# Performance work log

Measured on AMD Instinct MI355X. Metric: run time of the kernel, lower is better.

## Reference

```python
import jax, jax.numpy as jnp
import numpy as np

B, D_IN, D_OUT, Q, NUM_CLASSES = 256, 512, 256, 16, 100
POOL = 2  # patch_size = sqrt(n=4) -> 2x2 spatial mean pooling


def setup_inputs() -> dict:
    key = jax.random.key(0)
    k1, k2, k3 = jax.random.split(key, 3)
    X = jax.random.normal(k1, (B, D_IN, Q), jnp.float32)
    # FRMap weight init: randn(d_out, d_in) / sqrt(d_in)
    W = jax.random.normal(k2, (D_OUT, D_IN), jnp.float32) / np.sqrt(D_IN)
    d2 = D_OUT // POOL
    fc_w = jax.random.normal(k3, (NUM_CLASSES, d2 * d2), jnp.float32) / np.sqrt(d2 * d2)
    fc_b = jnp.zeros((NUM_CLASSES,), jnp.float32)
    return {"X": X, "W": W, "fc_w": fc_w, "fc_b": fc_b}


def reference(X, W, fc_w, fc_b):
    # FRMap: Y = W @ X  -> (B, d_out, q)
    Y = jnp.einsum('oi,biq->boq', W, X)
    # ReOrth: Q from reduced QR of Y -> orthonormal (B, d_out, q)
    Qm, _ = jnp.linalg.qr(Y)
    # ProjMap: P = Q Q^T -> (B, d_out, d_out)
    P = jnp.einsum('biq,bjq->bij', Qm, Qm)
    # ProjPooling (spatial, n=4): 2x2 mean pooling == adaptive_avg_pool2d to (d/2, d/2)
    b, d, _ = P.shape
    d2 = d // POOL
    Pp = P.reshape(b, d2, POOL, d2, POOL).mean(axis=(2, 4))  # (B, d2, d2)
    # OrthMap: top-q eigenvectors of symmetric Pp (eigh ascending -> take last q, descending)
    _, V = jnp.linalg.eigh(Pp)
    U = V[..., ::-1][..., :Q]  # (B, d2, q)
    # OutputBlock: ProjMap + flatten + FC
    P2 = jnp.einsum('biq,bjq->bij', U, U)  # (B, d2, d2)
    logits = P2.reshape(b, -1) @ fc_w.T + fc_b  # (B, num_classes)
    return logits
```

## Files before the change

### kernel.cpp

```cpp
#include <hip/hip_runtime.h>
#include <hip/hip_bf16.h>
#include <cstdint>

#define BATCH 256
#define DIN   512
#define D2    128
#define NQ    16
#define NC    100
#define KFC   (D2 * D2)

#define KS    32
#define KCH   (KFC / KS)
#define STEPS (KCH / 32)

#define ZPAD  132
#define CVT_BLKS  800
#define W2_BLKS   256
#define BIAS_BLKS 100

typedef short short8 __attribute__((ext_vector_type(8)));
typedef float f32x4  __attribute__((ext_vector_type(4)));
typedef float f32x16 __attribute__((ext_vector_type(16)));

static __device__ __forceinline__ unsigned short f2bf_rne(float f) {
    unsigned x = __float_as_uint(f);
    return (unsigned short)((x + 0x7fffu + ((x >> 16) & 1u)) >> 16);
}
static __device__ __forceinline__ float bf2f(unsigned short u) {
    return __uint_as_float(((unsigned)u) << 16);
}

__global__ __launch_bounds__(256) void k_prep(const float* __restrict__ W,
                                              const float* __restrict__ fcw,
                                              const float* __restrict__ fcb,
                                              __hip_bfloat16* __restrict__ W2hi,
                                              __hip_bfloat16* __restrict__ W2lo,
                                              __hip_bfloat16* __restrict__ fcw16,
                                              float* __restrict__ out) {
    int blk = blockIdx.x;
    if (blk < CVT_BLKS) {
        int i = (blk * 256 + threadIdx.x) * 8;
        float4 a = *(const float4*)(fcw + i);
        float4 b = *(const float4*)(fcw + i + 4);
        short8 v;
        __hip_bfloat16* h = (__hip_bfloat16*)&v;
        h[0] = __float2bfloat16(a.x); h[1] = __float2bfloat16(a.y);
        h[2] = __float2bfloat16(a.z); h[3] = __float2bfloat16(a.w);
        h[4] = __float2bfloat16(b.x); h[5] = __float2bfloat16(b.y);
        h[6] = __float2bfloat16(b.z); h[7] = __float2bfloat16(b.w);
        *(short8*)(fcw16 + i) = v;
    } else if (blk < CVT_BLKS + W2_BLKS) {
        int idx = (blk - CVT_BLKS) * 256 + threadIdx.x;
        int o = idx >> 9;
        int i = idx & (DIN - 1);
        float v = 0.5f * (W[(size_t)(2 * o) * DIN + i] +
                          W[(size_t)(2 * o + 1) * DIN + i]);
        unsigned short hi = f2bf_rne(v);
        unsigned short lo = f2bf_rne(v - bf2f(hi));
        *(unsigned short*)(W2hi + idx) = hi;
        *(unsigned short*)(W2lo + idx) = lo;
    } else {
        int idx = (blk - CVT_BLKS - W2_BLKS) * 256 + threadIdx.x;
        int c = idx % NC;
        out[idx] = fcb[c];
    }
}

#define GJ_STEP(K) do {                                                   \
    float piv = __shfl(g[(K) & 7], ((K) >> 3) * 16 + (K), 64);            \
    float fac = __shfl(g[(K) & 7], ((K) >> 3) * 16 + r, 64);              \
    float inv = 1.0f / piv;                                               \
    float f   = fac * inv;                                                \
    float p0 = __shfl(g[0], cg16 + (K), 64);                              \
    float p1 = __shfl(g[1], cg16 + (K), 64);                              \
    float p2 = __shfl(g[2], cg16 + (K), 64);                              \
    float p3 = __shfl(g[3], cg16 + (K), 64);                              \
    float p4 = __shfl(g[4], cg16 + (K), 64);                              \
    float p5 = __shfl(g[5], cg16 + (K), 64);                              \
    float p6 = __shfl(g[6], cg16 + (K), 64);                              \
    float p7 = __shfl(g[7], cg16 + (K), 64);                              \
    bool isk = (r == (K));                                                \
    g[0] = isk ? p0 * inv : fmaf(-f, p0, g[0]);                           \
    g[1] = isk ? p1 * inv : fmaf(-f, p1, g[1]);                           \
    g[2] = isk ? p2 * inv : fmaf(-f, p2, g[2]);                           \
    g[3] = isk ? p3 * inv : fmaf(-f, p3, g[3]);                           \
    g[4] = isk ? p4 * inv : fmaf(-f, p4, g[4]);                           \
    g[5] = isk ? p5 * inv : fmaf(-f, p5, g[5]);                           \
    g[6] = isk ? p6 * inv : fmaf(-f, p6, g[6]);                           \
    g[7] = isk ? p7 * inv : fmaf(-f, p7, g[7]);                           \
} while (0)

__global__ __launch_bounds__(512) void k_zgep(const float* __restrict__ X,
                                              const __hip_bfloat16* __restrict__ W2hi,
                                              const __hip_bfloat16* __restrict__ W2lo,
                                              __hip_bfloat16* __restrict__ P2) {
    __shared__ float Xs[DIN][17];
    __shared__ unsigned int FragHi[16 * 256];
    __shared__ unsigned int FragLo[16 * 256];
    __shared__ float Zt[NQ][ZPAD];
    __shared__ float Et[NQ][ZPAD];
    __shared__ float Gi[NQ][36];

    int b = blockIdx.x;
    int t = threadIdx.x;
    int l = t & 63;
    int wv = t >> 6;

    {
        const float4* src = (const float4*)(X + (size_t)b * DIN * NQ);
        #pragma unroll
        for (int r = 0; r < 4; ++r) {
            float4 v = src[t + r * 512];
            int idx = (t + r * 512) * 4;
            int i = idx >> 4, q = idx & 15;
            Xs[i][q]     = v.x;
            Xs[i][q + 1] = v.y;
            Xs[i][q + 2] = v.z;
            Xs[i][q + 3] = v.w;
        }
    }
    __syncthreads();

    #pragma unroll
    for (int it = 0; it < 8; ++it) {
        int d  = t + it * 512;
        int s  = d >> 8;
        int ln = (d >> 2) & 63;
        int jj = d & 3;
        int q  = ln & 15;
        int i0 = s * 32 + ((ln >> 4) & 3) * 8 + jj * 2;
        float v0 = Xs[i0][q], v1 = Xs[i0 + 1][q];
        unsigned short h0 = f2bf_rne(v0), h1 = f2bf_rne(v1);
        unsigned short l0 = f2bf_rne(v0 - bf2f(h0));
        unsigned short l1 = f2bf_rne(v1 - bf2f(h1));
        FragHi[d] = (unsigned)h0 | ((unsigned)h1 << 16);
        FragLo[d] = (unsigned)l0 | ((unsigned)l1 << 16);
    }
    __syncthreads();

    {
        int m  = l & 15;
        int kg = (l >> 4) * 8;
        const __hip_bfloat16* whi = W2hi + (size_t)(wv * 16 + m) * DIN + kg;
        const __hip_bfloat16* wlo = W2lo + (size_t)(wv * 16 + m) * DIN + kg;
        f32x4 acc = {0.f, 0.f, 0.f, 0.f};
        #pragma unroll 4
        for (int s = 0; s < 16; ++s) {
            short8 ahi = *(const short8*)(whi + s * 32);
            short8 alo = *(const short8*)(wlo + s * 32);
            short8 bhi = *(const short8*)(&FragHi[s * 256 + l * 4]);
            short8 blo = *(const short8*)(&FragLo[s * 256 + l * 4]);
            acc = __builtin_amdgcn_mfma_f32_16x16x32_bf16(ahi, bhi, acc, 0, 0, 0);
            acc = __builtin_amdgcn_mfma_f32_16x16x32_bf16(ahi, blo, acc, 0, 0, 0);
            acc = __builtin_amdgcn_mfma_f32_16x16x32_bf16(alo, bhi, acc, 0, 0, 0);
        }
        int r0 = (l >> 4) * 4;
        #pragma unroll
        for (int j = 0; j < 4; ++j)
            Zt[m][wv * 16 + r0 + j] = acc[j];
    }
    __syncthreads();

    if (t < 256) {
        int qq = t >> 4, rr = t & 15;
        float s = 0.f;
        for (int i = 0; i < D2; i += 4) {
            float4 a = *(const float4*)&Zt[qq][i];
            float4 c = *(const float4*)&Zt[rr][i];
            s = fmaf(a.x, c.x, s); s = fmaf(a.y, c.y, s);
            s = fmaf(a.z, c.z, s); s = fmaf(a.w, c.w, s);
        }
        Gi[qq][rr] = s;
        Gi[qq][NQ + rr] = (qq == rr) ? 1.f : 0.f;
    }
    __syncthreads();

    if (t < 64) {
        int r    = t & 15;
        int cgg  = t >> 4;
        int cg16 = cgg * 16;
        float g[8];
        #pragma unroll
        for (int j = 0; j < 8; ++j) g[j] = Gi[r][cgg * 8 + j];
        GJ_STEP(0);  GJ_STEP(1);  GJ_STEP(2);  GJ_STEP(3);
        GJ_STEP(4);  GJ_STEP(5);  GJ_STEP(6);  GJ_STEP(7);
        GJ_STEP(8);  GJ_STEP(9);  GJ_STEP(10); GJ_STEP(11);
        GJ_STEP(12); GJ_STEP(13); GJ_STEP(14); GJ_STEP(15);
        if (cgg >= 2) {
            #pragma unroll
            for (int j = 0; j < 8; ++j) Gi[r][cgg * 8 + j] = g[j];
        }
    }
    __syncthreads();

    {
        int o  = t & (D2 - 1);
        int qg = (t >> 7) * 4;
        float acc[4] = {};
        #pragma unroll
        for (int rp = 0; rp < NQ; ++rp) {
            float z = Zt[rp][o];
            #pragma unroll
            for (int j = 0; j < 4; ++j)
                acc[j] = fmaf(z, Gi[rp][NQ + qg + j], acc[j]);
        }
        #pragma unroll
        for (int j = 0; j < 4; ++j) Et[qg + j][o] = acc[j];
    }
    __syncthreads();

    {
        __hip_bfloat16* P2b = P2 + (size_t)b * KFC;
        int ti = wv >> 1;
        int tj0 = (wv & 1) * 2;
        int r8 = (l >> 5) * 8;
        int rm = l & 31;

        short8 afr;
        {
            __hip_bfloat16* ah = (__hip_bfloat16*)&afr;
            #pragma unroll
            for (int j = 0; j < 8; ++j)
                ah[j] = __float2bfloat16(Et[r8 + j][ti * 32 + rm]);
        }
        #pragma unroll
        for (int tjo = 0; tjo < 2; ++tjo) {
            int tj = tj0 + tjo;
            short8 bfr;
            __hip_bfloat16* bh = (__hip_bfloat16*)&bfr;
            #pragma unroll
            for (int j = 0; j < 8; ++j)
                bh[j] = __float2bfloat16(Zt[r8 + j][tj * 32 + rm]);
            f32x16 cc = {};
            cc = __builtin_amdgcn_mfma_f32_32x32x16_bf16(afr, bfr, cc, 0, 0, 0);
            #pragma unroll
            for (int reg = 0; reg < 16; ++reg) {
                int row = (reg & 3) + 8 * (reg >> 2) + 4 * (l >> 5);
                P2b[(size_t)(ti * 32 + row) * D2 + tj * 32 + rm] =
                    __float2bfloat16(cc[reg]);
            }
        }
    }
}

__global__ __launch_bounds__(256) void k_fc(const __hip_bfloat16* __restrict__ P2,
                                            const __hip_bfloat16* __restrict__ fcw16,
                                            float* __restrict__ out) {
    int bt = blockIdx.x;
    int ks = blockIdx.y;
    int t  = threadIdx.x;
    int lane = t & 63;
    int w    = t >> 6;
    int m  = lane & 15;
    int kg = (lane >> 4) * 8;

    const __hip_bfloat16* pa =
        P2 + (size_t)(bt * 16 + m) * KFC + ks * KCH + kg;

    int c0 = w * 32 + m;
    int c1 = c0 + 16;
    bool v0 = (c0 < NC), v1 = (c1 < NC);
    const __hip_bfloat16* pb0 =
        fcw16 + (size_t)(v0 ? c0 : 0) * KFC + ks * KCH + kg;
    const __hip_bfloat16* pb1 =
        fcw16 + (size_t)(v1 ? c1 : 0) * KFC + ks * KCH + kg;

    f32x4 acc0 = {0.f, 0.f, 0.f, 0.f};
    f32x4 acc1 = {0.f, 0.f, 0.f, 0.f};
    short8 zz = {};

    #pragma unroll 4
    for (int s = 0; s < STEPS; ++s) {
        short8 a  = *(const short8*)(pa + s * 32);
        short8 b0 = v0 ? *(const short8*)(pb0 + s * 32) : zz;
        short8 b1 = v1 ? *(const short8*)(pb1 + s * 32) : zz;
        acc0 = __builtin_amdgcn_mfma_f32_16x16x32_bf16(a, b0, acc0, 0, 0, 0);
        acc1 = __builtin_amdgcn_mfma_f32_16x16x32_bf16(a, b1, acc1, 0, 0, 0);
    }

    int r0 = (lane >> 4) * 4;
    int b0 = bt * 16 + r0;
    #pragma unroll
    for (int j = 0; j < 4; ++j) {
        if (v0) atomicAdd(&out[(size_t)(b0 + j) * NC + c0], acc0[j]);
        if (v1) atomicAdd(&out[(size_t)(b0 + j) * NC + c1], acc1[j]);
    }
}

extern "C" void kernel_launch(void* const* d_in, const int* in_sizes, int n_in,
                              void* d_out, int out_size, void* d_ws, size_t ws_size,
                              hipStream_t stream) {
    const float* X   = (const float*)d_in[0];
    const float* W   = (const float*)d_in[1];
    const float* fcw = (const float*)d_in[2];
    const float* fcb = (const float*)d_in[3];
    float* out = (float*)d_out;

    __hip_bfloat16* W2hi  = (__hip_bfloat16*)d_ws;
    __hip_bfloat16* W2lo  = W2hi + 65536;
    __hip_bfloat16* fcw16 = W2lo + 65536;
    __hip_bfloat16* P2b16 = fcw16 + 1638400;

    k_prep<<<dim3(CVT_BLKS + W2_BLKS + BIAS_BLKS), 256, 0, stream>>>(
        W, fcw, fcb, W2hi, W2lo, fcw16, out);
    k_zgep<<<dim3(BATCH), 512, 0, stream>>>(X, W2hi, W2lo, P2b16);
    k_fc  <<<dim3(16, KS), 256, 0, stream>>>(P2b16, fcw16, out);
}
```

Measured before the change: 43.97 us.

## Fold weight precision conversion and bias init into consumer kernels, drop prep kernel

```diff
diff --git a/kernel.cpp b/kernel.cpp
--- a/kernel.cpp
+++ b/kernel.cpp
@@ -14,9 +14,6 @@
 #define STEPS (KCH / 32)
 
 #define ZPAD  132
-#define CVT_BLKS  800
-#define W2_BLKS   256
-#define BIAS_BLKS 100
 
 typedef short short8 __attribute__((ext_vector_type(8)));
 typedef float f32x4  __attribute__((ext_vector_type(4)));
@@ -28,42 +25,6 @@
 }
 static __device__ __forceinline__ float bf2f(unsigned short u) {
     return __uint_as_float(((unsigned)u) << 16);
-}
-
-__global__ __launch_bounds__(256) void k_prep(const float* __restrict__ W,
-                                              const float* __restrict__ fcw,
-                                              const float* __restrict__ fcb,
-                                              __hip_bfloat16* __restrict__ W2hi,
-                                              __hip_bfloat16* __restrict__ W2lo,
-                                              __hip_bfloat16* __restrict__ fcw16,
-                                              float* __restrict__ out) {
-    int blk = blockIdx.x;
-    if (blk < CVT_BLKS) {
-        int i = (blk * 256 + threadIdx.x) * 8;
-        float4 a = *(const float4*)(fcw + i);
-        float4 b = *(const float4*)(fcw + i + 4);
-        short8 v;
-        __hip_bfloat16* h = (__hip_bfloat16*)&v;
-        h[0] = __float2bfloat16(a.x); h[1] = __float2bfloat16(a.y);
-        h[2] = __float2bfloat16(a.z); h[3] = __float2bfloat16(a.w);
-        h[4] = __float2bfloat16(b.x); h[5] = __float2bfloat16(b.y);
-        h[6] = __float2bfloat16(b.z); h[7] = __float2bfloat16(b.w);
-        *(short8*)(fcw16 + i) = v;
-    } else if (blk < CVT_BLKS + W2_BLKS) {
-        int idx = (blk - CVT_BLKS) * 256 + threadIdx.x;
-        int o = idx >> 9;
-        int i = idx & (DIN - 1);
-        float v = 0.5f * (W[(size_t)(2 * o) * DIN + i] +
-                          W[(size_t)(2 * o + 1) * DIN + i]);
-        unsigned short hi = f2bf_rne(v);
-        unsigned short lo = f2bf_rne(v - bf2f(hi));
-        *(unsigned short*)(W2hi + idx) = hi;
-        *(unsigned short*)(W2lo + idx) = lo;
-    } else {
-        int idx = (blk - CVT_BLKS - W2_BLKS) * 256 + threadIdx.x;
-        int c = idx % NC;
-        out[idx] = fcb[c];
-    }
 }
 
 #define GJ_STEP(K) do {                                                   \
@@ -91,9 +52,10 @@
 } while (0)
 
 __global__ __launch_bounds__(512) void k_zgep(const float* __restrict__ X,
-                                              const __hip_bfloat16* __restrict__ W2hi,
-                                              const __hip_bfloat16* __restrict__ W2lo,
-                                              __hip_bfloat16* __restrict__ P2) {
+                                              const float* __restrict__ W,
+                                              const float* __restrict__ fcb,
+                                              __hip_bfloat16* __restrict__ P2,
+                                              float* __restrict__ out) {
     __shared__ float Xs[DIN][17];
     __shared__ unsigned int FragHi[16 * 256];
     __shared__ unsigned int FragLo[16 * 256];
@@ -105,6 +67,8 @@
     int t = threadIdx.x;
     int l = t & 63;
     int wv = t >> 6;
+
+    if (t < NC) out[(size_t)b * NC + t] = fcb[t];
 
     {
         const float4* src = (const float4*)(X + (size_t)b * DIN * NQ);
@@ -141,13 +105,30 @@
     {
         int m  = l & 15;
         int kg = (l >> 4) * 8;
-        const __hip_bfloat16* whi = W2hi + (size_t)(wv * 16 + m) * DIN + kg;
-        const __hip_bfloat16* wlo = W2lo + (size_t)(wv * 16 + m) * DIN + kg;
+        int o  = wv * 16 + m;
+        const float* w0 = W + (size_t)(2 * o) * DIN + kg;
+        const float* w1 = W + (size_t)(2 * o + 1) * DIN + kg;
         f32x4 acc = {0.f, 0.f, 0.f, 0.f};
         #pragma unroll 4
         for (int s = 0; s < 16; ++s) {
-            short8 ahi = *(const short8*)(whi + s * 32);
-            short8 alo = *(const short8*)(wlo + s * 32);
+            float4 x0 = *(const float4*)(w0 + s * 32);
+            float4 x1 = *(const float4*)(w0 + s * 32 + 4);
+            float4 y0 = *(const float4*)(w1 + s * 32);
+            float4 y1 = *(const float4*)(w1 + s * 32 + 4);
+            float va[8];
+            va[0] = 0.5f * (x0.x + y0.x); va[1] = 0.5f * (x0.y + y0.y);
+            va[2] = 0.5f * (x0.z + y0.z); va[3] = 0.5f * (x0.w + y0.w);
+            va[4] = 0.5f * (x1.x + y1.x); va[5] = 0.5f * (x1.y + y1.y);
+            va[6] = 0.5f * (x1.z + y1.z); va[7] = 0.5f * (x1.w + y1.w);
+            short8 ahi, alo;
+            unsigned short* hh = (unsigned short*)&ahi;
+            unsigned short* ll = (unsigned short*)&alo;
+            #pragma unroll
+            for (int j = 0; j < 8; ++j) {
+                unsigned short h = f2bf_rne(va[j]);
+                hh[j] = h;
+                ll[j] = f2bf_rne(va[j] - bf2f(h));
+            }
             short8 bhi = *(const short8*)(&FragHi[s * 256 + l * 4]);
             short8 blo = *(const short8*)(&FragLo[s * 256 + l * 4]);
             acc = __builtin_amdgcn_mfma_f32_16x16x32_bf16(ahi, bhi, acc, 0, 0, 0);
@@ -218,19 +199,19 @@
 
         short8 afr;
         {
-            __hip_bfloat16* ah = (__hip_bfloat16*)&afr;
+            unsigned short* ah = (unsigned short*)&afr;
             #pragma unroll
             for (int j = 0; j < 8; ++j)
-                ah[j] = __float2bfloat16(Et[r8 + j][ti * 32 + rm]);
+                ah[j] = f2bf_rne(Et[r8 + j][ti * 32 + rm]);
         }
         #pragma unroll
         for (int tjo = 0; tjo < 2; ++tjo) {
             int tj = tj0 + tjo;
             short8 bfr;
-            __hip_bfloat16* bh = (__hip_bfloat16*)&bfr;
+            unsigned short* bh = (unsigned short*)&bfr;
             #pragma unroll
             for (int j = 0; j < 8; ++j)
-                bh[j] = __float2bfloat16(Zt[r8 + j][tj * 32 + rm]);
+                bh[j] = f2bf_rne(Zt[r8 + j][tj * 32 + rm]);
             f32x16 cc = {};
             cc = __builtin_amdgcn_mfma_f32_32x32x16_bf16(afr, bfr, cc, 0, 0, 0);
             #pragma unroll
@@ -244,7 +225,7 @@
 }
 
 __global__ __launch_bounds__(256) void k_fc(const __hip_bfloat16* __restrict__ P2,
-                                            const __hip_bfloat16* __restrict__ fcw16,
+                                            const float* __restrict__ fcw,
                                             float* __restrict__ out) {
     int bt = blockIdx.x;
     int ks = blockIdx.y;
@@ -260,30 +241,44 @@
     int c0 = w * 32 + m;
     int c1 = c0 + 16;
     bool v0 = (c0 < NC), v1 = (c1 < NC);
-    const __hip_bfloat16* pb0 =
-        fcw16 + (size_t)(v0 ? c0 : 0) * KFC + ks * KCH + kg;
-    const __hip_bfloat16* pb1 =
-        fcw16 + (size_t)(v1 ? c1 : 0) * KFC + ks * KCH + kg;
+    const float* pb0 = fcw + (size_t)(v0 ? c0 : 0) * KFC + ks * KCH + kg;
+    const float* pb1 = fcw + (size_t)(v1 ? c1 : 0) * KFC + ks * KCH + kg;
 
     f32x4 acc0 = {0.f, 0.f, 0.f, 0.f};
     f32x4 acc1 = {0.f, 0.f, 0.f, 0.f};
-    short8 zz = {};
 
     #pragma unroll 4
     for (int s = 0; s < STEPS; ++s) {
-        short8 a  = *(const short8*)(pa + s * 32);
-        short8 b0 = v0 ? *(const short8*)(pb0 + s * 32) : zz;
-        short8 b1 = v1 ? *(const short8*)(pb1 + s * 32) : zz;
+        short8 a = *(const short8*)(pa + s * 32);
+        short8 b0 = {}, b1 = {};
+        if (v0) {
+            float4 f0 = *(const float4*)(pb0 + s * 32);
+            float4 f1 = *(const float4*)(pb0 + s * 32 + 4);
+            unsigned short* h = (unsigned short*)&b0;
+            h[0] = f2bf_rne(f0.x); h[1] = f2bf_rne(f0.y);
+            h[2] = f2bf_rne(f0.z); h[3] = f2bf_rne(f0.w);
+            h[4] = f2bf_rne(f1.x); h[5] = f2bf_rne(f1.y);
+            h[6] = f2bf_rne(f1.z); h[7] = f2bf_rne(f1.w);
+        }
+        if (v1) {
+            float4 f0 = *(const float4*)(pb1 + s * 32);
+            float4 f1 = *(const float4*)(pb1 + s * 32 + 4);
+            unsigned short* h = (unsigned short*)&b1;
+            h[0] = f2bf_rne(f0.x); h[1] = f2bf_rne(f0.y);
+            h[2] = f2bf_rne(f0.z); h[3] = f2bf_rne(f0.w);
+            h[4] = f2bf_rne(f1.x); h[5] = f2bf_rne(f1.y);
+            h[6] = f2bf_rne(f1.z); h[7] = f2bf_rne(f1.w);
+        }
         acc0 = __builtin_amdgcn_mfma_f32_16x16x32_bf16(a, b0, acc0, 0, 0, 0);
         acc1 = __builtin_amdgcn_mfma_f32_16x16x32_bf16(a, b1, acc1, 0, 0, 0);
     }
 
     int r0 = (lane >> 4) * 4;
-    int b0 = bt * 16 + r0;
+    int b0r = bt * 16 + r0;
     #pragma unroll
     for (int j = 0; j < 4; ++j) {
-        if (v0) atomicAdd(&out[(size_t)(b0 + j) * NC + c0], acc0[j]);
-        if (v1) atomicAdd(&out[(size_t)(b0 + j) * NC + c1], acc1[j]);
+        if (v0) atomicAdd(&out[(size_t)(b0r + j) * NC + c0], acc0[j]);
+        if (v1) atomicAdd(&out[(size_t)(b0r + j) * NC + c1], acc1[j]);
     }
 }
 
@@ -296,13 +291,8 @@
     const float* fcb = (const float*)d_in[3];
     float* out = (float*)d_out;
 
-    __hip_bfloat16* W2hi  = (__hip_bfloat16*)d_ws;
-    __hip_bfloat16* W2lo  = W2hi + 65536;
-    __hip_bfloat16* fcw16 = W2lo + 65536;
-    __hip_bfloat16* P2b16 = fcw16 + 1638400;
-
-    k_prep<<<dim3(CVT_BLKS + W2_BLKS + BIAS_BLKS), 256, 0, stream>>>(
-        W, fcw, fcb, W2hi, W2lo, fcw16, out);
-    k_zgep<<<dim3(BATCH), 512, 0, stream>>>(X, W2hi, W2lo, P2b16);
-    k_fc  <<<dim3(16, KS), 256, 0, stream>>>(P2b16, fcw16, out);
-}
+    __hip_bfloat16* P2b16 = (__hip_bfloat16*)d_ws;
+
+    k_zgep<<<dim3(BATCH), 512, 0, stream>>>(X, W, fcb, P2b16, out);
+    k_fc  <<<dim3(16, KS), 256, 0, stream>>>(P2b16, fcw, out);
+}
```

New measurement: 50.37 us. 1.15x slower.
